# Kernel tuning notes

Hardware: AMD Instinct MI355X
Metric: run time of the kernel (lower is better)

The kernel has to match this reference:

```python
import jax, jax.numpy as jnp
import numpy as np

EPS = 1e-5

def conv3x3(x, w, b):
    # x: [B,C,H,W], w: [O,I,3,3] -> SAME padding (pad=1)
    y = jax.lax.conv_general_dilated(x, w, (1, 1), 'SAME',
                                     dimension_numbers=('NCHW', 'OIHW', 'NCHW'))
    return y + b[None, :, None, None]

def batchnorm(x, g, b):
    # training-mode batch statistics over (B,H,W), biased variance (torch default)
    m = x.mean(axis=(0, 2, 3), keepdims=True)
    v = x.var(axis=(0, 2, 3), keepdims=True)
    return (x - m) / jnp.sqrt(v + EPS) * g[None, :, None, None] + b[None, :, None, None]

def setup_inputs() -> dict:
    key = jax.random.key(0)
    ks = jax.random.split(key, 24)
    B, Cin, Cout, T, H, W = 16, 256, 256, 256, 32, 32
    Cq = Cout // 8
    s = lambda fan: 1.0 / np.sqrt(fan)
    inp = {
        'x': jax.random.normal(ks[0], (B, Cin, H, W), jnp.float32),
        't': jax.random.normal(ks[1], (B, T), jnp.float32),
        # time_mlp: Linear(T,T) -> ReLU -> Linear(T,Cout)
        'w_t1': jax.random.normal(ks[2], (T, T), jnp.float32) * s(T),
        'b_t1': jax.random.normal(ks[3], (T,), jnp.float32) * s(T),
        'w_t2': jax.random.normal(ks[4], (Cout, T), jnp.float32) * s(T),
        'b_t2': jax.random.normal(ks[5], (Cout,), jnp.float32) * s(T),
        # convs (3x3, pad=1)
        'w_c1': jax.random.normal(ks[6], (Cout, Cin, 3, 3), jnp.float32) * s(Cin * 9),
        'b_c1': jax.random.normal(ks[7], (Cout,), jnp.float32) * s(Cin * 9),
        'w_c2': jax.random.normal(ks[8], (Cout, Cout, 3, 3), jnp.float32) * s(Cout * 9),
        'b_c2': jax.random.normal(ks[9], (Cout,), jnp.float32) * s(Cout * 9),
        'w_tr': jax.random.normal(ks[10], (Cout, Cout, 3, 3), jnp.float32) * s(Cout * 9),
        'b_tr': jax.random.normal(ks[11], (Cout,), jnp.float32) * s(Cout * 9),
        # batchnorm affine params
        'bn1_g': jnp.ones((Cout,), jnp.float32),
        'bn1_b': jnp.zeros((Cout,), jnp.float32),
        'bn2_g': jnp.ones((Cout,), jnp.float32),
        'bn2_b': jnp.zeros((Cout,), jnp.float32),
        # self-attention 1x1 convs (stored as [O,I])
        'wq': jax.random.normal(ks[12], (Cq, Cout), jnp.float32) * s(Cout),
        'bq': jax.random.normal(ks[13], (Cq,), jnp.float32) * s(Cout),
        'wk': jax.random.normal(ks[14], (Cq, Cout), jnp.float32) * s(Cout),
        'bk': jax.random.normal(ks[15], (Cq,), jnp.float32) * s(Cout),
        'wv': jax.random.normal(ks[16], (Cout, Cout), jnp.float32) * s(Cout),
        'bv': jax.random.normal(ks[17], (Cout,), jnp.float32) * s(Cout),
        # gamma is nn.Parameter(zeros(1)); use a random value so the residual branch is exercised
        'gamma': jax.random.normal(ks[18], (1,), jnp.float32),
    }
    return inp

def reference(x, t, w_t1, b_t1, w_t2, b_t2, w_c1, b_c1, w_c2, b_c2, w_tr, b_tr,
              bn1_g, bn1_b, bn2_g, bn2_b, wq, bq, wk, bk, wv, bv, gamma):
    # --- Block ---
    h = batchnorm(jax.nn.relu(conv3x3(x, w_c1, b_c1)), bn1_g, bn1_b)
    te = jax.nn.relu(t @ w_t1.T + b_t1)
    te = jax.nn.relu(te @ w_t2.T + b_t2)          # [B, Cout]
    h = h + te[:, :, None, None]
    h = batchnorm(jax.nn.relu(conv3x3(h, w_c2, b_c2)), bn2_g, bn2_b)
    y = conv3x3(h, w_tr, b_tr)                    # transform (up=False)
    # --- SelfAttention ---
    B, C, H, W = y.shape
    yf = y.reshape(B, C, H * W)                   # [B, C, N]
    Q = jnp.einsum('qc,bcn->bnq', wq, yf) + bq[None, None, :]   # [B, N, Cq]
    K = jnp.einsum('qc,bcn->bqn', wk, yf) + bk[None, :, None]   # [B, Cq, N]
    V = jnp.einsum('vc,bcn->bvn', wv, yf) + bv[None, :, None]   # [B, C, N]
    attn = jax.nn.softmax(jnp.einsum('bnq,bqm->bnm', Q, K), axis=-1)  # [B, N, N]
    out = jnp.einsum('bcm,bnm->bcn', V, attn).reshape(B, C, H, W)
    return gamma[0] * out + y
```

## Files before the change

### kernel.cpp

```cpp
#include <hip/hip_runtime.h>
#include <hip/hip_bf16.h>

using bf16 = __hip_bfloat16;

typedef __attribute__((ext_vector_type(8))) short bf16x8_t;
typedef __attribute__((ext_vector_type(4))) float f32x4_t;

__device__ __forceinline__ float b2f(bf16 x){ return __bfloat162float(x); }
__device__ __forceinline__ bf16  f2b(float x){ return __float2bfloat16(x); }
__device__ __forceinline__ unsigned short f2bu(float x){ bf16 h = __float2bfloat16(x); return *(unsigned short*)&h; }
__device__ __forceinline__ float bits2f(unsigned int lo16){ return __uint_as_float(lo16 << 16); }

__device__ __forceinline__ void gload16(const void* g, void* l) {
    __builtin_amdgcn_global_load_lds(
        (const __attribute__((address_space(1))) unsigned int*)g,
        (__attribute__((address_space(3))) unsigned int*)l, 16, 0, 0);
}


__global__ void zero_k(unsigned int* __restrict__ p, unsigned int n) {
    for (unsigned int i = blockIdx.x * 256 + threadIdx.x; i < n; i += gridDim.x * 256) p[i] = 0u;
}

__global__ __launch_bounds__(256) void time_mlp_k(
    const float* __restrict__ t, const float* __restrict__ w1, const float* __restrict__ b1,
    const float* __restrict__ w2, const float* __restrict__ b2, float* __restrict__ te)
{
    const int b = blockIdx.x, j = threadIdx.x;
    __shared__ float tr[256], hid[256];
    tr[j] = t[(b << 8) + j];
    __syncthreads();
    float s = b1[j];
    const float* wp = w1 + j * 256;
    for (int k = 0; k < 256; ++k) s += tr[k] * wp[k];
    hid[j] = fmaxf(s, 0.f);
    __syncthreads();
    float s2 = b2[j];
    const float* wp2 = w2 + j * 256;
    for (int k = 0; k < 256; ++k) s2 += hid[k] * wp2[k];
    te[(b << 8) + j] = fmaxf(s2, 0.f);
}

__global__ __launch_bounds__(256) void prep_w_all_k(
    const float* __restrict__ w1, const float* __restrict__ w2, const float* __restrict__ w3,
    bf16* __restrict__ W1, bf16* __restrict__ W2, bf16* __restrict__ W3o)
{
    __shared__ float ls[2304];
    const int t = threadIdx.x;
    const int co = blockIdx.x & 255;
    const int sel = blockIdx.x >> 8;
    const float* w = (sel == 0) ? w1 : (sel == 1) ? w2 : w3;
    bf16* dst = (sel == 0) ? W1 : (sel == 1) ? W2 : W3o;
    const float* src = w + (size_t)co * 2304;
    #pragma unroll
    for (int i = 0; i < 9; ++i) ls[t + (i << 8)] = src[t + (i << 8)];
    __syncthreads();
    #pragma unroll
    for (int off = 0; off < 9; ++off)
        dst[(size_t)(co * 9 + off) * 256 + t] = f2b(ls[t * 9 + off]);
}

__global__ __launch_bounds__(256) void prep_wqkv_k(
    const float* __restrict__ wq, const float* __restrict__ wk, const float* __restrict__ wv,
    bf16* __restrict__ WQK, bf16* __restrict__ WVb)
{
    const int r = blockIdx.x, c = threadIdx.x;
    if (r < 32)       WQK[r * 256 + c] = f2b(wq[r * 256 + c]);
    else if (r < 64)  WQK[r * 256 + c] = f2b(wk[(r - 32) * 256 + c]);
    else              WVb[(r - 64) * 256 + c] = f2b(wv[(r - 64) * 256 + c]);
}

__global__ __launch_bounds__(256) void prep_x_k(const float* __restrict__ x, bf16* __restrict__ Xp,
                                                float* __restrict__ sums)
{
    __shared__ float xs[64][65];
    const int t = threadIdx.x;
    if (blockIdx.x == 0) {
        sums[t] = 0.f; sums[t + 256] = 0.f; sums[t + 512] = 0.f; sums[t + 768] = 0.f;
    }
    const int b = blockIdx.x >> 6, ct = (blockIdx.x >> 4) & 3, nt = blockIdx.x & 15;
    const int c0 = ct << 6, n0 = nt << 6;
    {
        const int cl = t >> 2, nc = (t & 3) << 4;
        const float* src = x + (size_t)((b << 8) + c0 + cl) * 1024 + n0 + nc;
        #pragma unroll
        for (int j = 0; j < 16; j += 4) {
            const float4 v = *(const float4*)(src + j);
            xs[cl][nc + j] = v.x; xs[cl][nc + j + 1] = v.y;
            xs[cl][nc + j + 2] = v.z; xs[cl][nc + j + 3] = v.w;
        }
    }
    __syncthreads();
    {
        const int nl = t >> 2, cc = (t & 3) << 4;
        const int n = n0 + nl;
        const int p = ((n >> 5) + 1) * 34 + (n & 31) + 1;
        unsigned int u[8];
        #pragma unroll
        for (int k = 0; k < 8; ++k)
            u[k] = (unsigned int)f2bu(xs[cc + 2 * k][nl]) | ((unsigned int)f2bu(xs[cc + 2 * k + 1][nl]) << 16);
        bf16* dst = Xp + (size_t)(b * 1156 + p) * 256 + c0 + cc;
        *(uint4*)dst = make_uint4(u[0], u[1], u[2], u[3]);
        *(uint4*)(dst + 8) = make_uint4(u[4], u[5], u[6], u[7]);
    }
}

template<bool RELU, bool STATS>
__global__ __launch_bounds__(512, 1) void conv_mfma_k(
    const bf16* __restrict__ Xp, const bf16* __restrict__ W3,
    const float* __restrict__ bias, bf16* __restrict__ outp, float* __restrict__ sums)
{
    __shared__ bf16 Als[3][128 * 64];
    __shared__ bf16 Bls[3][128 * 64];
    __shared__ float sstat[256];
    const int tid = threadIdx.x;
    const int wid = tid >> 6, lane = tid & 63;
    const int wm = wid >> 2, wn = wid & 3;
    const int blk = blockIdx.x;
    const int xc = blk & 7, tt = blk >> 3;
    const int b = xc + ((tt >> 4) << 3);
    const int tile = tt & 15, mt = tile >> 1, nt = tile & 1;
    const int m0 = mt << 7, co0 = nt << 7;

    if (STATS && tid < 256) sstat[tid] = 0.f;

    const int lrow = tid >> 3;
    const int sL8 = (((tid & 7) ^ (lrow & 7)) << 3);

    const bf16* agp[2]; const bf16* bgp[2];
    #pragma unroll
    for (int i = 0; i < 2; ++i) {
        const int r = (i << 6) + lrow;
        const int n = m0 + r;
        const int pb = (n >> 5) * 34 + (n & 31);
        agp[i] = Xp + (size_t)(b * 1156 + pb) * 256 + sL8;
        bgp[i] = W3 + (size_t)(co0 + r) * 2304 + sL8;
    }

    const int rsel = lane & 15;
    const int s0 = (((lane >> 4) ^ (lane & 7)) << 3);
    const int s1 = ((((lane >> 4) + 4) ^ (lane & 7)) << 3);
    const int abase = ((wm << 6) + rsel) << 6;
    const int bbase = ((wn << 5) + rsel) << 6;

    f32x4_t acc[4][2];
    #pragma unroll
    for (int mi = 0; mi < 4; ++mi)
        #pragma unroll
        for (int ni = 0; ni < 2; ++ni)
            acc[mi][ni] = (f32x4_t){0.f, 0.f, 0.f, 0.f};

    auto STAGE = [&](int kt2, int buf) {
        const int off_ = kt2 >> 2, cic_ = kt2 & 3;
        const int kh_ = (off_ * 11) >> 5;
        const int doff_ = ((off_ + 31 * kh_) << 8) + (cic_ << 6);
        const int koff_ = (off_ << 8) + (cic_ << 6);
        #pragma unroll
        for (int i = 0; i < 2; ++i) {
            gload16(agp[i] + doff_, &Als[buf][((i << 6) + (wid << 3)) << 6]);
            gload16(bgp[i] + koff_, &Bls[buf][((i << 6) + (wid << 3)) << 6]);
        }
    };

    STAGE(0, 0); STAGE(1, 1);
    for (int kt = 0; kt < 36; ++kt) {
        if (kt < 35) asm volatile("s_waitcnt vmcnt(4)" ::: "memory");
        else         asm volatile("s_waitcnt vmcnt(0)" ::: "memory");
        __builtin_amdgcn_s_barrier();
        asm volatile("" ::: "memory");
        const int cur = kt % 3;
        #pragma unroll
        for (int kh = 0; kh < 2; ++kh) {
            const int sk = kh ? s1 : s0;
            bf16x8_t av[4], bv[2];
            #pragma unroll
            for (int mi = 0; mi < 4; ++mi)
                av[mi] = *(const bf16x8_t*)(&Als[cur][abase + (mi << 10) + sk]);
            #pragma unroll
            for (int ni = 0; ni < 2; ++ni)
                bv[ni] = *(const bf16x8_t*)(&Bls[cur][bbase + (ni << 10) + sk]);
            #pragma unroll
            for (int mi = 0; mi < 4; ++mi)
                #pragma unroll
                for (int ni = 0; ni < 2; ++ni)
                    acc[mi][ni] = __builtin_amdgcn_mfma_f32_16x16x32_bf16(
                        av[mi], bv[ni], acc[mi][ni], 0, 0, 0);
        }
        if (kt + 2 < 36) STAGE(kt + 2, (kt + 2) % 3);
    }

    const int cr = (lane >> 4) << 2;
    const int cc = lane & 15;
    #pragma unroll
    for (int ni = 0; ni < 2; ++ni) {
        const int co = co0 + (wn << 5) + (ni << 4) + cc;
        const float bb = bias[co];
        float ssum = 0.f, ssq = 0.f;
        #pragma unroll
        for (int mi = 0; mi < 4; ++mi) {
            const int n = m0 + (wm << 6) + (mi << 4) + cr;
            #pragma unroll
            for (int j = 0; j < 4; ++j) {
                float v = acc[mi][ni][j] + bb;
                if (RELU) v = fmaxf(v, 0.f);
                outp[(size_t)((b << 10) + n + j) * 256 + co] = f2b(v);
                if (STATS) { ssum += v; ssq += v * v; }
            }
        }
        if (STATS) {
            ssum += __shfl_xor(ssum, 16); ssum += __shfl_xor(ssum, 32);
            ssq  += __shfl_xor(ssq, 16);  ssq  += __shfl_xor(ssq, 32);
            if (lane < 16) {
                const int ch = (wn << 5) + (ni << 4) + cc;
                atomicAdd(&sstat[ch * 2], ssum);
                atomicAdd(&sstat[ch * 2 + 1], ssq);
            }
        }
    }
    if (STATS) {
        __syncthreads();
        if (tid < 128) {
            atomicAdd(&sums[co0 + tid], sstat[tid * 2]);
            atomicAdd(&sums[256 + co0 + tid], sstat[tid * 2 + 1]);
        }
    }
}

template<bool TE>
__global__ __launch_bounds__(256) void bn_apply_T_k(
    const bf16* __restrict__ a, const float* __restrict__ sums,
    const float* __restrict__ g, const float* __restrict__ bb,
    const float* __restrict__ te, bf16* __restrict__ Xp)
{
    const int t = threadIdx.x;
    const int row = blockIdx.x * 8 + (t >> 5);
    const int c0 = (t & 31) << 3;
    const int b = row >> 10, n = row & 1023;
    const uint4 u = *(const uint4*)(a + (size_t)row * 256 + c0);
    const unsigned int w[4] = {u.x, u.y, u.z, u.w};
    float scv[8], shv[8];
    #pragma unroll
    for (int k = 0; k < 8; ++k) {
        const int c = c0 + k;
        const float m = sums[c] * (1.f / 16384.f);
        const float var = sums[256 + c] * (1.f / 16384.f) - m * m;
        const float sc = g[c] * rsqrtf(var + 1e-5f);
        scv[k] = sc;
        shv[k] = bb[c] - m * sc + (TE ? te[(b << 8) + c] : 0.f);
    }
    unsigned int o[4];
    #pragma unroll
    for (int k = 0; k < 4; ++k) {
        const float v0 = bits2f(w[k] & 0xffffu) * scv[2*k] + shv[2*k];
        const float v1 = __uint_as_float(w[k] & 0xffff0000u) * scv[2*k+1] + shv[2*k+1];
        o[k] = (unsigned int)f2bu(v0) | ((unsigned int)f2bu(v1) << 16);
    }
    const int p = ((n >> 5) + 1) * 34 + (n & 31) + 1;
    *(uint4*)(Xp + (size_t)(b * 1156 + p) * 256 + c0) = make_uint4(o[0], o[1], o[2], o[3]);
}

__global__ __launch_bounds__(256) void qk_mfma_k(
    const bf16* __restrict__ Yt, const bf16* __restrict__ WQK,
    const float* __restrict__ bq, const float* __restrict__ bk, bf16* __restrict__ QKb)
{
    const int b = blockIdx.x >> 4, m0 = (blockIdx.x & 15) << 6;
    const int tid = threadIdx.x, wid = tid >> 6, lane = tid & 63;
    const int n0w = m0 + (wid << 4);
    const bf16* arow = Yt + (size_t)((b << 10) + n0w + (lane & 15)) * 256 + ((lane >> 4) << 3);
    const int boff = ((lane >> 4) << 3);
    f32x4_t acc[4];
    #pragma unroll
    for (int ni = 0; ni < 4; ++ni) acc[ni] = (f32x4_t){0.f,0.f,0.f,0.f};
    for (int k0 = 0; k0 < 256; k0 += 32) {
        const bf16x8_t av = *(const bf16x8_t*)(arow + k0);
        #pragma unroll
        for (int ni = 0; ni < 4; ++ni) {
            const bf16x8_t bv = *(const bf16x8_t*)(WQK + (ni * 16 + (lane & 15)) * 256 + k0 + boff);
            acc[ni] = __builtin_amdgcn_mfma_f32_16x16x32_bf16(av, bv, acc[ni], 0, 0, 0);
        }
    }
    const int cr = (lane >> 4) << 2, cc = lane & 15;
    #pragma unroll
    for (int ni = 0; ni < 4; ++ni) {
        const int q = ni * 16 + cc;
        const float bias = (q < 32) ? bq[q] : bk[q - 32];
        #pragma unroll
        for (int j = 0; j < 4; ++j) {
            const int n = n0w + cr + j;
            QKb[(size_t)((b << 10) + n) * 64 + q] = f2b(acc[ni][j] + bias);
        }
    }
}

__global__ __launch_bounds__(512, 1) void v_mfma_k(
    const bf16* __restrict__ WVb, const bf16* __restrict__ Yt,
    const float* __restrict__ bvp, bf16* __restrict__ Vb)
{
    __shared__ bf16 Als[3][128 * 64];
    __shared__ bf16 Bls[3][128 * 64];
    const int tid = threadIdx.x;
    const int wid = tid >> 6, lane = tid & 63;
    const int wm = wid >> 2, wn = wid & 3;
    const int blk = blockIdx.x;
    const int xc = blk & 7, tt = blk >> 3;
    const int b = xc + ((tt >> 4) << 3);
    const int tile = tt & 15, vt = tile >> 3, nt = tile & 7;
    const int v0 = vt << 7, n0 = nt << 7;

    const int lrow = tid >> 3;
    const int sL8 = (((tid & 7) ^ (lrow & 7)) << 3);
    const bf16* agp[2]; const bf16* bgp[2];
    #pragma unroll
    for (int i = 0; i < 2; ++i) {
        const int r = (i << 6) + lrow;
        agp[i] = WVb + (size_t)(v0 + r) * 256 + sL8;
        bgp[i] = Yt + (size_t)((b << 10) + n0 + r) * 256 + sL8;
    }
    const int rsel = lane & 15;
    const int s0 = (((lane >> 4) ^ (lane & 7)) << 3);
    const int s1 = ((((lane >> 4) + 4) ^ (lane & 7)) << 3);
    const int abase = ((wm << 6) + rsel) << 6;
    const int bbase = ((wn << 5) + rsel) << 6;

    f32x4_t acc[4][2];
    #pragma unroll
    for (int mi = 0; mi < 4; ++mi)
        #pragma unroll
        for (int ni = 0; ni < 2; ++ni)
            acc[mi][ni] = (f32x4_t){0.f,0.f,0.f,0.f};

    auto STAGE = [&](int kt2, int buf) {
        const int koff = kt2 << 6;
        #pragma unroll
        for (int i = 0; i < 2; ++i) {
            gload16(agp[i] + koff, &Als[buf][((i << 6) + (wid << 3)) << 6]);
            gload16(bgp[i] + koff, &Bls[buf][((i << 6) + (wid << 3)) << 6]);
        }
    };

    STAGE(0, 0); STAGE(1, 1);
    for (int kt = 0; kt < 4; ++kt) {
        if (kt < 3) asm volatile("s_waitcnt vmcnt(4)" ::: "memory");
        else        asm volatile("s_waitcnt vmcnt(0)" ::: "memory");
        __builtin_amdgcn_s_barrier();
        asm volatile("" ::: "memory");
        const int cur = kt % 3;
        #pragma unroll
        for (int kh = 0; kh < 2; ++kh) {
            const int sk = kh ? s1 : s0;
            bf16x8_t av[4], bv[2];
            #pragma unroll
            for (int mi = 0; mi < 4; ++mi)
                av[mi] = *(const bf16x8_t*)(&Als[cur][abase + (mi << 10) + sk]);
            #pragma unroll
            for (int ni = 0; ni < 2; ++ni)
                bv[ni] = *(const bf16x8_t*)(&Bls[cur][bbase + (ni << 10) + sk]);
            #pragma unroll
            for (int mi = 0; mi < 4; ++mi)
                #pragma unroll
                for (int ni = 0; ni < 2; ++ni)
                    acc[mi][ni] = __builtin_amdgcn_mfma_f32_16x16x32_bf16(
                        av[mi], bv[ni], acc[mi][ni], 0, 0, 0);
        }
        if (kt + 2 < 4) STAGE(kt + 2, (kt + 2) % 3);
    }

    const int cr = (lane >> 4) << 2, cc = lane & 15;
    #pragma unroll
    for (int mi = 0; mi < 4; ++mi) {
        #pragma unroll
        for (int j = 0; j < 4; ++j) {
            const int v = v0 + (wm << 6) + (mi << 4) + cr + j;
            const float bb = bvp[v];
            #pragma unroll
            for (int ni = 0; ni < 2; ++ni) {
                const int n = n0 + (wn << 5) + (ni << 4) + cc;
                Vb[(size_t)((b << 8) + v) * 1024 + n] = f2b(acc[mi][ni][j] + bb);
            }
        }
    }
}

__global__ __launch_bounds__(256) void softmax_k(
    const bf16* __restrict__ QKb, bf16* __restrict__ P, float* __restrict__ invs)
{
    const int b = blockIdx.x >> 5, n0 = (blockIdx.x & 31) << 5;
    const int tid = threadIdx.x, wid = tid >> 6, lane = tid & 63;
    const int m0w = wid << 8;
    __shared__ float wred[4][32];

    const bf16* qbase = QKb + (size_t)((b << 10) + n0) * 64;
    const int koff = (lane >> 4) << 3;
    bf16x8_t qf[2];
    #pragma unroll
    for (int nt = 0; nt < 2; ++nt)
        qf[nt] = *(const bf16x8_t*)(qbase + (nt * 16 + (lane & 15)) * 64 + koff);
    const bf16* kbase = QKb + (size_t)(b << 10) * 64 + 32;

    float mx[2] = {-3.0e38f, -3.0e38f};
    for (int mi = 0; mi < 16; ++mi) {
        const bf16x8_t kf = *(const bf16x8_t*)(kbase + (m0w + mi * 16 + (lane & 15)) * 64 + koff);
        #pragma unroll
        for (int nt = 0; nt < 2; ++nt) {
            f32x4_t s = (f32x4_t){0.f,0.f,0.f,0.f};
            s = __builtin_amdgcn_mfma_f32_16x16x32_bf16(kf, qf[nt], s, 0, 0, 0);
            mx[nt] = fmaxf(mx[nt], fmaxf(fmaxf(s[0], s[1]), fmaxf(s[2], s[3])));
        }
    }
    #pragma unroll
    for (int nt = 0; nt < 2; ++nt) {
        mx[nt] = fmaxf(mx[nt], __shfl_xor(mx[nt], 16));
        mx[nt] = fmaxf(mx[nt], __shfl_xor(mx[nt], 32));
        if (lane < 16) wred[wid][nt * 16 + lane] = mx[nt];
    }
    __syncthreads();
    float rm[2];
    #pragma unroll
    for (int nt = 0; nt < 2; ++nt) {
        const int c = nt * 16 + (lane & 15);
        rm[nt] = fmaxf(fmaxf(wred[0][c], wred[1][c]), fmaxf(wred[2][c], wred[3][c]));
    }
    __syncthreads();

    float sm[2] = {0.f, 0.f};
    for (int mi = 0; mi < 16; ++mi) {
        const bf16x8_t kf = *(const bf16x8_t*)(kbase + (m0w + mi * 16 + (lane & 15)) * 64 + koff);
        #pragma unroll
        for (int nt = 0; nt < 2; ++nt) {
            f32x4_t s = (f32x4_t){0.f,0.f,0.f,0.f};
            s = __builtin_amdgcn_mfma_f32_16x16x32_bf16(kf, qf[nt], s, 0, 0, 0);
            const float p0 = __expf(s[0] - rm[nt]);
            const float p1 = __expf(s[1] - rm[nt]);
            const float p2 = __expf(s[2] - rm[nt]);
            const float p3 = __expf(s[3] - rm[nt]);
            sm[nt] += (p0 + p1) + (p2 + p3);
            uint2 u;
            u.x = (unsigned int)f2bu(p0) | ((unsigned int)f2bu(p1) << 16);
            u.y = (unsigned int)f2bu(p2) | ((unsigned int)f2bu(p3) << 16);
            const int n = n0 + nt * 16 + (lane & 15);
            const int m = m0w + mi * 16 + ((lane >> 4) << 2);
            *(uint2*)(P + (size_t)((b << 10) + n) * 1024 + m) = u;
        }
    }
    #pragma unroll
    for (int nt = 0; nt < 2; ++nt) {
        sm[nt] += __shfl_xor(sm[nt], 16);
        sm[nt] += __shfl_xor(sm[nt], 32);
        if (lane < 16) wred[wid][nt * 16 + lane] = sm[nt];
    }
    __syncthreads();
    if (tid < 32) {
        const float total = wred[0][tid] + wred[1][tid] + wred[2][tid] + wred[3][tid];
        invs[(b << 10) + n0 + tid] = 1.f / total;
    }
}

__global__ __launch_bounds__(512, 1) void pv_mfma_k(
    const bf16* __restrict__ Vb, const bf16* __restrict__ P,
    const float* __restrict__ invs, const bf16* __restrict__ Yt,
    const float* __restrict__ gamma, float* __restrict__ out)
{
    __shared__ bf16 Als[3][128 * 64];
    __shared__ bf16 Bls[3][128 * 64];
    const int tid = threadIdx.x;
    const int wid = tid >> 6, lane = tid & 63;
    const int wm = wid >> 2, wn = wid & 3;
    const int blk = blockIdx.x;
    const int xc = blk & 7, tt = blk >> 3;
    const int b = xc + ((tt >> 4) << 3);
    const int tile = tt & 15, ct = tile >> 3, nt = tile & 7;
    const int c0 = ct << 7, n0 = nt << 7;

    const int lrow = tid >> 3;
    const int sL8 = (((tid & 7) ^ (lrow & 7)) << 3);
    const bf16* agp[2]; const bf16* bgp[2];
    #pragma unroll
    for (int i = 0; i < 2; ++i) {
        const int r = (i << 6) + lrow;
        agp[i] = Vb + (size_t)((b << 8) + c0 + r) * 1024 + sL8;
        bgp[i] = P + (size_t)((b << 10) + n0 + r) * 1024 + sL8;
    }
    const int rsel = lane & 15;
    const int s0 = (((lane >> 4) ^ (lane & 7)) << 3);
    const int s1 = ((((lane >> 4) + 4) ^ (lane & 7)) << 3);
    const int abase = ((wm << 6) + rsel) << 6;
    const int bbase = ((wn << 5) + rsel) << 6;

    f32x4_t acc[4][2];
    #pragma unroll
    for (int mi = 0; mi < 4; ++mi)
        #pragma unroll
        for (int ni = 0; ni < 2; ++ni)
            acc[mi][ni] = (f32x4_t){0.f,0.f,0.f,0.f};

    auto STAGE = [&](int kt2, int buf) {
        const int koff = kt2 << 6;
        #pragma unroll
        for (int i = 0; i < 2; ++i) {
            gload16(agp[i] + koff, &Als[buf][((i << 6) + (wid << 3)) << 6]);
            gload16(bgp[i] + koff, &Bls[buf][((i << 6) + (wid << 3)) << 6]);
        }
    };

    STAGE(0, 0); STAGE(1, 1);
    for (int kt = 0; kt < 16; ++kt) {
        if (kt < 15) asm volatile("s_waitcnt vmcnt(4)" ::: "memory");
        else         asm volatile("s_waitcnt vmcnt(0)" ::: "memory");
        __builtin_amdgcn_s_barrier();
        asm volatile("" ::: "memory");
        const int cur = kt % 3;
        #pragma unroll
        for (int kh = 0; kh < 2; ++kh) {
            const int sk = kh ? s1 : s0;
            bf16x8_t av[4], bv[2];
            #pragma unroll
            for (int mi = 0; mi < 4; ++mi)
                av[mi] = *(const bf16x8_t*)(&Als[cur][abase + (mi << 10) + sk]);
            #pragma unroll
            for (int ni = 0; ni < 2; ++ni)
                bv[ni] = *(const bf16x8_t*)(&Bls[cur][bbase + (ni << 10) + sk]);
            #pragma unroll
            for (int mi = 0; mi < 4; ++mi)
                #pragma unroll
                for (int ni = 0; ni < 2; ++ni)
                    acc[mi][ni] = __builtin_amdgcn_mfma_f32_16x16x32_bf16(
                        av[mi], bv[ni], acc[mi][ni], 0, 0, 0);
        }
        if (kt + 2 < 16) STAGE(kt + 2, (kt + 2) % 3);
    }

    const float g = gamma[0];
    const int cr = (lane >> 4) << 2, cc = lane & 15;
    #pragma unroll
    for (int ni = 0; ni < 2; ++ni) {
        const int n = n0 + (wn << 5) + (ni << 4) + cc;
        const float gi = g * invs[(b << 10) + n];
        #pragma unroll
        for (int mi = 0; mi < 4; ++mi) {
            const int c = c0 + (wm << 6) + (mi << 4) + cr;
            const bf16* yp = Yt + (size_t)((b << 10) + n) * 256 + c;
            #pragma unroll
            for (int j = 0; j < 4; ++j)
                out[(size_t)((b << 8) + c + j) * 1024 + n] = gi * acc[mi][ni][j] + b2f(yp[j]);
        }
    }
}

extern "C" void kernel_launch(void* const* d_in, const int* in_sizes, int n_in,
                              void* d_out, int out_size, void* d_ws, size_t ws_size,
                              hipStream_t stream)
{
    const float* x     = (const float*)d_in[0];
    const float* t     = (const float*)d_in[1];
    const float* w_t1  = (const float*)d_in[2];
    const float* b_t1  = (const float*)d_in[3];
    const float* w_t2  = (const float*)d_in[4];
    const float* b_t2  = (const float*)d_in[5];
    const float* w_c1  = (const float*)d_in[6];
    const float* b_c1  = (const float*)d_in[7];
    const float* w_c2  = (const float*)d_in[8];
    const float* b_c2  = (const float*)d_in[9];
    const float* w_tr  = (const float*)d_in[10];
    const float* b_tr  = (const float*)d_in[11];
    const float* bn1g  = (const float*)d_in[12];
    const float* bn1b  = (const float*)d_in[13];
    const float* bn2g  = (const float*)d_in[14];
    const float* bn2b  = (const float*)d_in[15];
    const float* wq    = (const float*)d_in[16];
    const float* bq    = (const float*)d_in[17];
    const float* wk    = (const float*)d_in[18];
    const float* bk    = (const float*)d_in[19];
    const float* wv    = (const float*)d_in[20];
    const float* bv    = (const float*)d_in[21];
    const float* gamma = (const float*)d_in[22];
    float* out = (float*)d_out;

    char* ws = (char*)d_ws;
    float* te    = (float*)(ws + 0);
    float* sums1 = (float*)(ws + 16384);
    float* sums2 = (float*)(ws + 18432);
    char* base = ws + 32768;
    bf16* W3_1 = (bf16*)(base);
    bf16* W3_2 = (bf16*)(base + 1179648);
    bf16* W3_3 = (bf16*)(base + 2359296);
    bf16* Xp0  = (bf16*)(base + 3538944);
    bf16* Xp1  = (bf16*)(base + 13008896);
    bf16* Craw = (bf16*)(base + 22478848);
    bf16* P    = (bf16*)(base);
    bf16* Yt   = (bf16*)(base + 33554432);
    bf16* QKb  = (bf16*)(base + 41943040);
    bf16* Vb   = (bf16*)(base + 44040192);
    float* invs= (float*)(base + 52428800);
    bf16* WQK  = (bf16*)(base + 52494336);
    bf16* WVb  = (bf16*)(base + 52527104);

    const unsigned int XP2_U32 = 2u * 16u * 1156u * 256u / 2u;

    zero_k<<<2048, 256, 0, stream>>>((unsigned int*)Xp0, XP2_U32);
    time_mlp_k<<<16, 256, 0, stream>>>(t, w_t1, b_t1, w_t2, b_t2, te);
    prep_w_all_k<<<768, 256, 0, stream>>>(w_c1, w_c2, w_tr, W3_1, W3_2, W3_3);
    prep_wqkv_k<<<320, 256, 0, stream>>>(wq, wk, wv, WQK, WVb);
    prep_x_k<<<1024, 256, 0, stream>>>(x, Xp0, sums1);

    conv_mfma_k<true, true><<<256, 512, 0, stream>>>(Xp0, W3_1, b_c1, Craw, sums1);
    bn_apply_T_k<true><<<2048, 256, 0, stream>>>(Craw, sums1, bn1g, bn1b, te, Xp1);

    conv_mfma_k<true, true><<<256, 512, 0, stream>>>(Xp1, W3_2, b_c2, Craw, sums2);
    bn_apply_T_k<false><<<2048, 256, 0, stream>>>(Craw, sums2, bn2g, bn2b, nullptr, Xp0);

    conv_mfma_k<false, false><<<256, 512, 0, stream>>>(Xp0, W3_3, b_tr, Yt, nullptr);

    qk_mfma_k<<<256, 256, 0, stream>>>(Yt, WQK, bq, bk, QKb);
    v_mfma_k<<<256, 512, 0, stream>>>(WVb, Yt, bv, Vb);
    softmax_k<<<512, 256, 0, stream>>>(QKb, P, invs);
    pv_mfma_k<<<256, 512, 0, stream>>>(Vb, P, invs, Yt, gamma, out);
}
```

Baseline: 169.7 us.

## Fuse softmax and PV matmul into flash-style online-softmax attention kernel

Replaces the separate softmax kernel, which wrote the full BxNxN probability matrix to global memory, and the PV matmul that read it back, with one kernel using online softmax. Each wave recomputes QK^T scores per 64-key chunk, rescales its running accumulator, stages probabilities through per-wave LDS and feeds them to MFMA against V loaded straight from global. This removes the P round trip (about 32MB of bf16) and one launch. In exchange, QK scores are recomputed by every channel-tile block (two C tiles per n tile), V is read from global without LDS staging or prefetch, and the exp and rescale work adds VALU load.

```diff
diff --git a/kernel.cpp b/kernel.cpp
--- a/kernel.cpp
+++ b/kernel.cpp
@@ -381,163 +381,139 @@
     }
 }
 
-__global__ __launch_bounds__(256) void softmax_k(
-    const bf16* __restrict__ QKb, bf16* __restrict__ P, float* __restrict__ invs)
-{
-    const int b = blockIdx.x >> 5, n0 = (blockIdx.x & 31) << 5;
-    const int tid = threadIdx.x, wid = tid >> 6, lane = tid & 63;
-    const int m0w = wid << 8;
-    __shared__ float wred[4][32];
-
-    const bf16* qbase = QKb + (size_t)((b << 10) + n0) * 64;
-    const int koff = (lane >> 4) << 3;
-    bf16x8_t qf[2];
-    #pragma unroll
-    for (int nt = 0; nt < 2; ++nt)
-        qf[nt] = *(const bf16x8_t*)(qbase + (nt * 16 + (lane & 15)) * 64 + koff);
-    const bf16* kbase = QKb + (size_t)(b << 10) * 64 + 32;
-
-    float mx[2] = {-3.0e38f, -3.0e38f};
-    for (int mi = 0; mi < 16; ++mi) {
-        const bf16x8_t kf = *(const bf16x8_t*)(kbase + (m0w + mi * 16 + (lane & 15)) * 64 + koff);
-        #pragma unroll
-        for (int nt = 0; nt < 2; ++nt) {
-            f32x4_t s = (f32x4_t){0.f,0.f,0.f,0.f};
-            s = __builtin_amdgcn_mfma_f32_16x16x32_bf16(kf, qf[nt], s, 0, 0, 0);
-            mx[nt] = fmaxf(mx[nt], fmaxf(fmaxf(s[0], s[1]), fmaxf(s[2], s[3])));
-        }
-    }
-    #pragma unroll
-    for (int nt = 0; nt < 2; ++nt) {
-        mx[nt] = fmaxf(mx[nt], __shfl_xor(mx[nt], 16));
-        mx[nt] = fmaxf(mx[nt], __shfl_xor(mx[nt], 32));
-        if (lane < 16) wred[wid][nt * 16 + lane] = mx[nt];
-    }
-    __syncthreads();
-    float rm[2];
-    #pragma unroll
-    for (int nt = 0; nt < 2; ++nt) {
-        const int c = nt * 16 + (lane & 15);
-        rm[nt] = fmaxf(fmaxf(wred[0][c], wred[1][c]), fmaxf(wred[2][c], wred[3][c]));
-    }
-    __syncthreads();
-
-    float sm[2] = {0.f, 0.f};
-    for (int mi = 0; mi < 16; ++mi) {
-        const bf16x8_t kf = *(const bf16x8_t*)(kbase + (m0w + mi * 16 + (lane & 15)) * 64 + koff);
-        #pragma unroll
-        for (int nt = 0; nt < 2; ++nt) {
-            f32x4_t s = (f32x4_t){0.f,0.f,0.f,0.f};
-            s = __builtin_amdgcn_mfma_f32_16x16x32_bf16(kf, qf[nt], s, 0, 0, 0);
-            const float p0 = __expf(s[0] - rm[nt]);
-            const float p1 = __expf(s[1] - rm[nt]);
-            const float p2 = __expf(s[2] - rm[nt]);
-            const float p3 = __expf(s[3] - rm[nt]);
-            sm[nt] += (p0 + p1) + (p2 + p3);
-            uint2 u;
-            u.x = (unsigned int)f2bu(p0) | ((unsigned int)f2bu(p1) << 16);
-            u.y = (unsigned int)f2bu(p2) | ((unsigned int)f2bu(p3) << 16);
-            const int n = n0 + nt * 16 + (lane & 15);
-            const int m = m0w + mi * 16 + ((lane >> 4) << 2);
-            *(uint2*)(P + (size_t)((b << 10) + n) * 1024 + m) = u;
-        }
-    }
-    #pragma unroll
-    for (int nt = 0; nt < 2; ++nt) {
-        sm[nt] += __shfl_xor(sm[nt], 16);
-        sm[nt] += __shfl_xor(sm[nt], 32);
-        if (lane < 16) wred[wid][nt * 16 + lane] = sm[nt];
-    }
-    __syncthreads();
-    if (tid < 32) {
-        const float total = wred[0][tid] + wred[1][tid] + wred[2][tid] + wred[3][tid];
-        invs[(b << 10) + n0 + tid] = 1.f / total;
-    }
-}
-
-__global__ __launch_bounds__(512, 1) void pv_mfma_k(
-    const bf16* __restrict__ Vb, const bf16* __restrict__ P,
-    const float* __restrict__ invs, const bf16* __restrict__ Yt,
-    const float* __restrict__ gamma, float* __restrict__ out)
-{
-    __shared__ bf16 Als[3][128 * 64];
-    __shared__ bf16 Bls[3][128 * 64];
+__global__ __launch_bounds__(512, 2) void attn_fused_k(
+    const bf16* __restrict__ QKb, const bf16* __restrict__ Vb,
+    const bf16* __restrict__ Yt, const float* __restrict__ gamma, float* __restrict__ out)
+{
+    __shared__ bf16 S_lds[8][2048];
     const int tid = threadIdx.x;
     const int wid = tid >> 6, lane = tid & 63;
+    const int l15 = lane & 15, lg = lane >> 4;
     const int wm = wid >> 2, wn = wid & 3;
     const int blk = blockIdx.x;
     const int xc = blk & 7, tt = blk >> 3;
     const int b = xc + ((tt >> 4) << 3);
     const int tile = tt & 15, ct = tile >> 3, nt = tile & 7;
-    const int c0 = ct << 7, n0 = nt << 7;
-
-    const int lrow = tid >> 3;
-    const int sL8 = (((tid & 7) ^ (lrow & 7)) << 3);
-    const bf16* agp[2]; const bf16* bgp[2];
-    #pragma unroll
-    for (int i = 0; i < 2; ++i) {
-        const int r = (i << 6) + lrow;
-        agp[i] = Vb + (size_t)((b << 8) + c0 + r) * 1024 + sL8;
-        bgp[i] = P + (size_t)((b << 10) + n0 + r) * 1024 + sL8;
-    }
-    const int rsel = lane & 15;
-    const int s0 = (((lane >> 4) ^ (lane & 7)) << 3);
-    const int s1 = ((((lane >> 4) + 4) ^ (lane & 7)) << 3);
-    const int abase = ((wm << 6) + rsel) << 6;
-    const int bbase = ((wn << 5) + rsel) << 6;
-
+    const int c0w = (ct << 7) + (wm << 6);
+    const int n0w = (nt << 7) + (wn << 5);
+
+    bf16* sl = S_lds[wid];
+    const int e0 = (l15 & 7) << 1;
+
+    bf16x8_t qf[2];
+    #pragma unroll
+    for (int ni = 0; ni < 2; ++ni)
+        qf[ni] = *(const bf16x8_t*)(QKb + (size_t)((b << 10) + n0w + ni * 16 + l15) * 64 + (lg << 3));
+
+    float m_run[2] = {-3.0e38f, -3.0e38f};
+    float s_run[2] = {0.f, 0.f};
     f32x4_t acc[4][2];
     #pragma unroll
     for (int mi = 0; mi < 4; ++mi)
         #pragma unroll
         for (int ni = 0; ni < 2; ++ni)
-            acc[mi][ni] = (f32x4_t){0.f,0.f,0.f,0.f};
-
-    auto STAGE = [&](int kt2, int buf) {
-        const int koff = kt2 << 6;
-        #pragma unroll
-        for (int i = 0; i < 2; ++i) {
-            gload16(agp[i] + koff, &Als[buf][((i << 6) + (wid << 3)) << 6]);
-            gload16(bgp[i] + koff, &Bls[buf][((i << 6) + (wid << 3)) << 6]);
-        }
-    };
-
-    STAGE(0, 0); STAGE(1, 1);
-    for (int kt = 0; kt < 16; ++kt) {
-        if (kt < 15) asm volatile("s_waitcnt vmcnt(4)" ::: "memory");
-        else         asm volatile("s_waitcnt vmcnt(0)" ::: "memory");
-        __builtin_amdgcn_s_barrier();
-        asm volatile("" ::: "memory");
-        const int cur = kt % 3;
-        #pragma unroll
-        for (int kh = 0; kh < 2; ++kh) {
-            const int sk = kh ? s1 : s0;
-            bf16x8_t av[4], bv[2];
-            #pragma unroll
-            for (int mi = 0; mi < 4; ++mi)
-                av[mi] = *(const bf16x8_t*)(&Als[cur][abase + (mi << 10) + sk]);
-            #pragma unroll
-            for (int ni = 0; ni < 2; ++ni)
-                bv[ni] = *(const bf16x8_t*)(&Bls[cur][bbase + (ni << 10) + sk]);
+            acc[mi][ni] = (f32x4_t){0.f, 0.f, 0.f, 0.f};
+
+    const bf16* kbase = QKb + (size_t)(b << 10) * 64 + 32 + (lg << 3);
+    const bf16* vbase = Vb + (size_t)((b << 8) + c0w) * 1024 + (lg << 3);
+
+    for (int m0 = 0; m0 < 1024; m0 += 64) {
+        bf16x8_t kf[4], av[4][2];
+        #pragma unroll
+        for (int mi = 0; mi < 4; ++mi)
+            kf[mi] = *(const bf16x8_t*)(kbase + (size_t)(m0 + mi * 16 + l15) * 64);
+        #pragma unroll
+        for (int mi = 0; mi < 4; ++mi)
+            #pragma unroll
+            for (int ms = 0; ms < 2; ++ms)
+                av[mi][ms] = *(const bf16x8_t*)(vbase + (size_t)(mi * 16 + l15) * 1024 + m0 + ms * 32);
+
+        f32x4_t s[4][2];
+        #pragma unroll
+        for (int mi = 0; mi < 4; ++mi)
+            #pragma unroll
+            for (int ni = 0; ni < 2; ++ni) {
+                f32x4_t z = (f32x4_t){0.f, 0.f, 0.f, 0.f};
+                s[mi][ni] = __builtin_amdgcn_mfma_f32_16x16x32_bf16(kf[mi], qf[ni], z, 0, 0, 0);
+            }
+
+        #pragma unroll
+        for (int ni = 0; ni < 2; ++ni) {
+            float tm = s[0][ni][0];
+            #pragma unroll
+            for (int mi = 0; mi < 4; ++mi)
+                #pragma unroll
+                for (int j = 0; j < 4; ++j) tm = fmaxf(tm, s[mi][ni][j]);
+            tm = fmaxf(tm, __shfl_xor(tm, 16));
+            tm = fmaxf(tm, __shfl_xor(tm, 32));
+            const float nm = fmaxf(m_run[ni], tm);
+            const float f = __expf(m_run[ni] - nm);
+            m_run[ni] = nm;
+            #pragma unroll
+            for (int mi = 0; mi < 4; ++mi)
+                #pragma unroll
+                for (int j = 0; j < 4; ++j) acc[mi][ni][j] *= f;
+            float ls = 0.f;
+            #pragma unroll
+            for (int mi = 0; mi < 4; ++mi)
+                #pragma unroll
+                for (int j = 0; j < 4; ++j) {
+                    const float p = __expf(s[mi][ni][j] - nm);
+                    s[mi][ni][j] = p;
+                    ls += p;
+                }
+            ls += __shfl_xor(ls, 16);
+            ls += __shfl_xor(ls, 32);
+            s_run[ni] = s_run[ni] * f + ls;
+        }
+
+        #pragma unroll
+        for (int ni = 0; ni < 2; ++ni) {
+            const int n_local = ni * 16 + l15;
+            const int rowb = n_local << 7;
+            #pragma unroll
+            for (int mi = 0; mi < 4; ++mi) {
+                const int pg = ((mi << 2) + lg) ^ e0;
+                uint2 u;
+                u.x = (unsigned int)f2bu(s[mi][ni][0]) | ((unsigned int)f2bu(s[mi][ni][1]) << 16);
+                u.y = (unsigned int)f2bu(s[mi][ni][2]) | ((unsigned int)f2bu(s[mi][ni][3]) << 16);
+                *(uint2*)((char*)sl + rowb + (pg << 3)) = u;
+            }
+        }
+        asm volatile("s_waitcnt lgkmcnt(0)" ::: "memory");
+        __builtin_amdgcn_sched_barrier(0);
+
+        bf16x8_t bv[2][2];
+        #pragma unroll
+        for (int ni = 0; ni < 2; ++ni) {
+            const int n_local = ni * 16 + l15;
+            const int rowb = n_local << 7;
+            #pragma unroll
+            for (int ms = 0; ms < 2; ++ms) {
+                const int pg = ((ms << 3) + (lg << 1)) ^ e0;
+                bv[ni][ms] = *(const bf16x8_t*)((const char*)sl + rowb + (pg << 3));
+            }
+        }
+
+        #pragma unroll
+        for (int ms = 0; ms < 2; ++ms)
             #pragma unroll
             for (int mi = 0; mi < 4; ++mi)
                 #pragma unroll
                 for (int ni = 0; ni < 2; ++ni)
                     acc[mi][ni] = __builtin_amdgcn_mfma_f32_16x16x32_bf16(
-                        av[mi], bv[ni], acc[mi][ni], 0, 0, 0);
-        }
-        if (kt + 2 < 16) STAGE(kt + 2, (kt + 2) % 3);
+                        av[mi][ms], bv[ni][ms], acc[mi][ni], 0, 0, 0);
+        asm volatile("" ::: "memory");
     }
 
     const float g = gamma[0];
-    const int cr = (lane >> 4) << 2, cc = lane & 15;
     #pragma unroll
     for (int ni = 0; ni < 2; ++ni) {
-        const int n = n0 + (wn << 5) + (ni << 4) + cc;
-        const float gi = g * invs[(b << 10) + n];
+        const int n = n0w + ni * 16 + l15;
+        const float gi = g / s_run[ni];
         #pragma unroll
         for (int mi = 0; mi < 4; ++mi) {
-            const int c = c0 + (wm << 6) + (mi << 4) + cr;
+            const int c = c0w + mi * 16 + (lg << 2);
             const bf16* yp = Yt + (size_t)((b << 10) + n) * 256 + c;
             #pragma unroll
             for (int j = 0; j < 4; ++j)
@@ -586,11 +562,9 @@
     bf16* Xp0  = (bf16*)(base + 3538944);
     bf16* Xp1  = (bf16*)(base + 13008896);
     bf16* Craw = (bf16*)(base + 22478848);
-    bf16* P    = (bf16*)(base);
     bf16* Yt   = (bf16*)(base + 33554432);
     bf16* QKb  = (bf16*)(base + 41943040);
     bf16* Vb   = (bf16*)(base + 44040192);
-    float* invs= (float*)(base + 52428800);
     bf16* WQK  = (bf16*)(base + 52494336);
     bf16* WVb  = (bf16*)(base + 52527104);
 
@@ -612,6 +586,5 @@
 
     qk_mfma_k<<<256, 256, 0, stream>>>(Yt, WQK, bq, bk, QKb);
     v_mfma_k<<<256, 512, 0, stream>>>(WVb, Yt, bv, Vb);
-    softmax_k<<<512, 256, 0, stream>>>(QKb, P, invs);
-    pv_mfma_k<<<256, 512, 0, stream>>>(Vb, P, invs, Yt, gamma, out);
-}
+    attn_fused_k<<<256, 512, 0, stream>>>(QKb, Vb, Yt, gamma, out);
+}
```

After: 184.3 us. 1.09x slower.

## Merge prep kernels into one launch, zero only halo borders, fuse QK and V projections

Applied to the files above, without the earlier changes.

Folds the zeroing, time-MLP, weight conversion, QKV weight prep and input transpose into a single block-dispatched prep kernel. The full zeroing of both padded buffers is replaced by writes to only the halo border rows. The QK and V projection kernels are merged into one launch, with extra blocks doing QK at 512 threads. This cuts launch count and memory traffic, but it relies on the interior of Xp1 always being fully overwritten, and the QK blocks now carry the large shared-memory allocation of the V path, which may lower occupancy.

```diff
diff --git a/kernel.cpp b/kernel.cpp
--- a/kernel.cpp
+++ b/kernel.cpp
@@ -18,90 +18,101 @@
 }
 
 
-__global__ void zero_k(unsigned int* __restrict__ p, unsigned int n) {
-    for (unsigned int i = blockIdx.x * 256 + threadIdx.x; i < n; i += gridDim.x * 256) p[i] = 0u;
-}
-
-__global__ __launch_bounds__(256) void time_mlp_k(
-    const float* __restrict__ t, const float* __restrict__ w1, const float* __restrict__ b1,
-    const float* __restrict__ w2, const float* __restrict__ b2, float* __restrict__ te)
-{
-    const int b = blockIdx.x, j = threadIdx.x;
-    __shared__ float tr[256], hid[256];
-    tr[j] = t[(b << 8) + j];
-    __syncthreads();
-    float s = b1[j];
-    const float* wp = w1 + j * 256;
-    for (int k = 0; k < 256; ++k) s += tr[k] * wp[k];
-    hid[j] = fmaxf(s, 0.f);
-    __syncthreads();
-    float s2 = b2[j];
-    const float* wp2 = w2 + j * 256;
-    for (int k = 0; k < 256; ++k) s2 += hid[k] * wp2[k];
-    te[(b << 8) + j] = fmaxf(s2, 0.f);
-}
-
-__global__ __launch_bounds__(256) void prep_w_all_k(
+__global__ __launch_bounds__(256) void prep_all_k(
+    const float* __restrict__ x, bf16* __restrict__ Xp0, bf16* __restrict__ Xp1,
+    float* __restrict__ sums,
+    const float* __restrict__ t, const float* __restrict__ w_t1, const float* __restrict__ b_t1,
+    const float* __restrict__ w_t2, const float* __restrict__ b_t2, float* __restrict__ te,
     const float* __restrict__ w1, const float* __restrict__ w2, const float* __restrict__ w3,
-    bf16* __restrict__ W1, bf16* __restrict__ W2, bf16* __restrict__ W3o)
-{
-    __shared__ float ls[2304];
-    const int t = threadIdx.x;
-    const int co = blockIdx.x & 255;
-    const int sel = blockIdx.x >> 8;
-    const float* w = (sel == 0) ? w1 : (sel == 1) ? w2 : w3;
-    bf16* dst = (sel == 0) ? W1 : (sel == 1) ? W2 : W3o;
-    const float* src = w + (size_t)co * 2304;
-    #pragma unroll
-    for (int i = 0; i < 9; ++i) ls[t + (i << 8)] = src[t + (i << 8)];
-    __syncthreads();
-    #pragma unroll
-    for (int off = 0; off < 9; ++off)
-        dst[(size_t)(co * 9 + off) * 256 + t] = f2b(ls[t * 9 + off]);
-}
-
-__global__ __launch_bounds__(256) void prep_wqkv_k(
+    bf16* __restrict__ W1, bf16* __restrict__ W2, bf16* __restrict__ W3o,
     const float* __restrict__ wq, const float* __restrict__ wk, const float* __restrict__ wv,
     bf16* __restrict__ WQK, bf16* __restrict__ WVb)
 {
-    const int r = blockIdx.x, c = threadIdx.x;
-    if (r < 32)       WQK[r * 256 + c] = f2b(wq[r * 256 + c]);
-    else if (r < 64)  WQK[r * 256 + c] = f2b(wk[(r - 32) * 256 + c]);
-    else              WVb[(r - 64) * 256 + c] = f2b(wv[(r - 64) * 256 + c]);
-}
-
-__global__ __launch_bounds__(256) void prep_x_k(const float* __restrict__ x, bf16* __restrict__ Xp,
-                                                float* __restrict__ sums)
-{
-    __shared__ float xs[64][65];
-    const int t = threadIdx.x;
-    if (blockIdx.x == 0) {
-        sums[t] = 0.f; sums[t + 256] = 0.f; sums[t + 512] = 0.f; sums[t + 768] = 0.f;
-    }
-    const int b = blockIdx.x >> 6, ct = (blockIdx.x >> 4) & 3, nt = blockIdx.x & 15;
-    const int c0 = ct << 6, n0 = nt << 6;
-    {
-        const int cl = t >> 2, nc = (t & 3) << 4;
-        const float* src = x + (size_t)((b << 8) + c0 + cl) * 1024 + n0 + nc;
-        #pragma unroll
-        for (int j = 0; j < 16; j += 4) {
-            const float4 v = *(const float4*)(src + j);
-            xs[cl][nc + j] = v.x; xs[cl][nc + j + 1] = v.y;
-            xs[cl][nc + j + 2] = v.z; xs[cl][nc + j + 3] = v.w;
-        }
-    }
-    __syncthreads();
-    {
-        const int nl = t >> 2, cc = (t & 3) << 4;
-        const int n = n0 + nl;
-        const int p = ((n >> 5) + 1) * 34 + (n & 31) + 1;
-        unsigned int u[8];
-        #pragma unroll
-        for (int k = 0; k < 8; ++k)
-            u[k] = (unsigned int)f2bu(xs[cc + 2 * k][nl]) | ((unsigned int)f2bu(xs[cc + 2 * k + 1][nl]) << 16);
-        bf16* dst = Xp + (size_t)(b * 1156 + p) * 256 + c0 + cc;
-        *(uint4*)dst = make_uint4(u[0], u[1], u[2], u[3]);
-        *(uint4*)(dst + 8) = make_uint4(u[4], u[5], u[6], u[7]);
+    __shared__ char smem[64 * 65 * 4];
+    const int blk = blockIdx.x;
+    const int tid = threadIdx.x;
+
+    if (blk < 1024) {
+        float (*xs)[65] = (float(*)[65])smem;
+        if (blk == 0) {
+            sums[tid] = 0.f; sums[tid + 256] = 0.f; sums[tid + 512] = 0.f; sums[tid + 768] = 0.f;
+        }
+        const int b = blk >> 6, ct = (blk >> 4) & 3, nt = blk & 15;
+        const int c0 = ct << 6, n0 = nt << 6;
+        {
+            const int cl = tid >> 2, nc = (tid & 3) << 4;
+            const float* src = x + (size_t)((b << 8) + c0 + cl) * 1024 + n0 + nc;
+            #pragma unroll
+            for (int j = 0; j < 16; j += 4) {
+                const float4 v = *(const float4*)(src + j);
+                xs[cl][nc + j] = v.x; xs[cl][nc + j + 1] = v.y;
+                xs[cl][nc + j + 2] = v.z; xs[cl][nc + j + 3] = v.w;
+            }
+        }
+        __syncthreads();
+        {
+            const int nl = tid >> 2, cc = (tid & 3) << 4;
+            const int n = n0 + nl;
+            const int p = ((n >> 5) + 1) * 34 + (n & 31) + 1;
+            unsigned int u[8];
+            #pragma unroll
+            for (int k = 0; k < 8; ++k)
+                u[k] = (unsigned int)f2bu(xs[cc + 2 * k][nl]) | ((unsigned int)f2bu(xs[cc + 2 * k + 1][nl]) << 16);
+            bf16* dst = Xp0 + (size_t)(b * 1156 + p) * 256 + c0 + cc;
+            *(uint4*)dst = make_uint4(u[0], u[1], u[2], u[3]);
+            *(uint4*)(dst + 8) = make_uint4(u[4], u[5], u[6], u[7]);
+        }
+    } else if (blk < 1792) {
+        float* ls = (float*)smem;
+        const int id = blk - 1024;
+        const int co = id & 255;
+        const int sel = id >> 8;
+        const float* w = (sel == 0) ? w1 : (sel == 1) ? w2 : w3;
+        bf16* dst = (sel == 0) ? W1 : (sel == 1) ? W2 : W3o;
+        const float* src = w + (size_t)co * 2304;
+        #pragma unroll
+        for (int i = 0; i < 9; ++i) ls[tid + (i << 8)] = src[tid + (i << 8)];
+        __syncthreads();
+        #pragma unroll
+        for (int off = 0; off < 9; ++off)
+            dst[(size_t)(co * 9 + off) * 256 + tid] = f2b(ls[tid * 9 + off]);
+    } else if (blk < 2112) {
+        const int r = blk - 1792;
+        if (r < 32)       WQK[r * 256 + tid] = f2b(wq[r * 256 + tid]);
+        else if (r < 64)  WQK[r * 256 + tid] = f2b(wk[(r - 32) * 256 + tid]);
+        else              WVb[(r - 64) * 256 + tid] = f2b(wv[(r - 64) * 256 + tid]);
+    } else if (blk < 2128) {
+        float* tr = (float*)smem;
+        float* hid = tr + 256;
+        const int b = blk - 2112, j = tid;
+        tr[j] = t[(b << 8) + j];
+        __syncthreads();
+        float s = b_t1[j];
+        const float* wp = w_t1 + j * 256;
+        for (int k = 0; k < 256; ++k) s += tr[k] * wp[k];
+        hid[j] = fmaxf(s, 0.f);
+        __syncthreads();
+        float s2 = b_t2[j];
+        const float* wp2 = w_t2 + j * 256;
+        for (int k = 0; k < 256; ++k) s2 += hid[k] * wp2[k];
+        te[(b << 8) + j] = fmaxf(s2, 0.f);
+    } else {
+        const int idx = (blk - 2128) * 256 + tid;
+        const int v = idx >> 6;
+        const int o = (idx & 63) << 1;
+        if (v < 4224) {
+            const int buf = v / 2112;
+            const int rem = v - buf * 2112;
+            const int b = rem / 132;
+            const int h = rem - b * 132;
+            int p;
+            if (h < 34)        p = h;
+            else if (h < 68)   p = 1122 + (h - 34);
+            else if (h < 100)  p = (h - 68 + 1) * 34;
+            else               p = (h - 100 + 1) * 34 + 33;
+            unsigned int* dst = (unsigned int*)((buf ? Xp1 : Xp0) + (size_t)(b * 1156 + p) * 256);
+            dst[o] = 0u; dst[o + 1] = 0u;
+        }
     }
 }
 
@@ -259,47 +270,48 @@
     *(uint4*)(Xp + (size_t)(b * 1156 + p) * 256 + c0) = make_uint4(o[0], o[1], o[2], o[3]);
 }
 
-__global__ __launch_bounds__(256) void qk_mfma_k(
-    const bf16* __restrict__ Yt, const bf16* __restrict__ WQK,
-    const float* __restrict__ bq, const float* __restrict__ bk, bf16* __restrict__ QKb)
-{
-    const int b = blockIdx.x >> 4, m0 = (blockIdx.x & 15) << 6;
-    const int tid = threadIdx.x, wid = tid >> 6, lane = tid & 63;
-    const int n0w = m0 + (wid << 4);
-    const bf16* arow = Yt + (size_t)((b << 10) + n0w + (lane & 15)) * 256 + ((lane >> 4) << 3);
-    const int boff = ((lane >> 4) << 3);
-    f32x4_t acc[4];
-    #pragma unroll
-    for (int ni = 0; ni < 4; ++ni) acc[ni] = (f32x4_t){0.f,0.f,0.f,0.f};
-    for (int k0 = 0; k0 < 256; k0 += 32) {
-        const bf16x8_t av = *(const bf16x8_t*)(arow + k0);
-        #pragma unroll
-        for (int ni = 0; ni < 4; ++ni) {
-            const bf16x8_t bv = *(const bf16x8_t*)(WQK + (ni * 16 + (lane & 15)) * 256 + k0 + boff);
-            acc[ni] = __builtin_amdgcn_mfma_f32_16x16x32_bf16(av, bv, acc[ni], 0, 0, 0);
-        }
-    }
-    const int cr = (lane >> 4) << 2, cc = lane & 15;
-    #pragma unroll
-    for (int ni = 0; ni < 4; ++ni) {
-        const int q = ni * 16 + cc;
-        const float bias = (q < 32) ? bq[q] : bk[q - 32];
-        #pragma unroll
-        for (int j = 0; j < 4; ++j) {
-            const int n = n0w + cr + j;
-            QKb[(size_t)((b << 10) + n) * 64 + q] = f2b(acc[ni][j] + bias);
-        }
-    }
-}
-
-__global__ __launch_bounds__(512, 1) void v_mfma_k(
+__global__ __launch_bounds__(512, 1) void qkv_mfma_k(
     const bf16* __restrict__ WVb, const bf16* __restrict__ Yt,
-    const float* __restrict__ bvp, bf16* __restrict__ Vb)
+    const float* __restrict__ bvp, bf16* __restrict__ Vb,
+    const bf16* __restrict__ WQK, const float* __restrict__ bq,
+    const float* __restrict__ bk, bf16* __restrict__ QKb)
 {
     __shared__ bf16 Als[3][128 * 64];
     __shared__ bf16 Bls[3][128 * 64];
     const int tid = threadIdx.x;
     const int wid = tid >> 6, lane = tid & 63;
+
+    if (blockIdx.x >= 256) {
+        const int blk2 = blockIdx.x - 256;
+        const int b = blk2 >> 3, m0 = (blk2 & 7) << 7;
+        const int n0w = m0 + (wid << 4);
+        const bf16* arow = Yt + (size_t)((b << 10) + n0w + (lane & 15)) * 256 + ((lane >> 4) << 3);
+        const int boff = ((lane >> 4) << 3);
+        f32x4_t acc[4];
+        #pragma unroll
+        for (int ni = 0; ni < 4; ++ni) acc[ni] = (f32x4_t){0.f,0.f,0.f,0.f};
+        for (int k0 = 0; k0 < 256; k0 += 32) {
+            const bf16x8_t av = *(const bf16x8_t*)(arow + k0);
+            #pragma unroll
+            for (int ni = 0; ni < 4; ++ni) {
+                const bf16x8_t bv = *(const bf16x8_t*)(WQK + (ni * 16 + (lane & 15)) * 256 + k0 + boff);
+                acc[ni] = __builtin_amdgcn_mfma_f32_16x16x32_bf16(av, bv, acc[ni], 0, 0, 0);
+            }
+        }
+        const int cr = (lane >> 4) << 2, cc = lane & 15;
+        #pragma unroll
+        for (int ni = 0; ni < 4; ++ni) {
+            const int q = ni * 16 + cc;
+            const float bias = (q < 32) ? bq[q] : bk[q - 32];
+            #pragma unroll
+            for (int j = 0; j < 4; ++j) {
+                const int n = n0w + cr + j;
+                QKb[(size_t)((b << 10) + n) * 64 + q] = f2b(acc[ni][j] + bias);
+            }
+        }
+        return;
+    }
+
     const int wm = wid >> 2, wn = wid & 3;
     const int blk = blockIdx.x;
     const int xc = blk & 7, tt = blk >> 3;
@@ -594,13 +606,11 @@
     bf16* WQK  = (bf16*)(base + 52494336);
     bf16* WVb  = (bf16*)(base + 52527104);
 
-    const unsigned int XP2_U32 = 2u * 16u * 1156u * 256u / 2u;
-
-    zero_k<<<2048, 256, 0, stream>>>((unsigned int*)Xp0, XP2_U32);
-    time_mlp_k<<<16, 256, 0, stream>>>(t, w_t1, b_t1, w_t2, b_t2, te);
-    prep_w_all_k<<<768, 256, 0, stream>>>(w_c1, w_c2, w_tr, W3_1, W3_2, W3_3);
-    prep_wqkv_k<<<320, 256, 0, stream>>>(wq, wk, wv, WQK, WVb);
-    prep_x_k<<<1024, 256, 0, stream>>>(x, Xp0, sums1);
+    prep_all_k<<<3184, 256, 0, stream>>>(
+        x, Xp0, Xp1, sums1,
+        t, w_t1, b_t1, w_t2, b_t2, te,
+        w_c1, w_c2, w_tr, W3_1, W3_2, W3_3,
+        wq, wk, wv, WQK, WVb);
 
     conv_mfma_k<true, true><<<256, 512, 0, stream>>>(Xp0, W3_1, b_c1, Craw, sums1);
     bn_apply_T_k<true><<<2048, 256, 0, stream>>>(Craw, sums1, bn1g, bn1b, te, Xp1);
@@ -610,8 +620,7 @@
 
     conv_mfma_k<false, false><<<256, 512, 0, stream>>>(Xp0, W3_3, b_tr, Yt, nullptr);
 
-    qk_mfma_k<<<256, 256, 0, stream>>>(Yt, WQK, bq, bk, QKb);
-    v_mfma_k<<<256, 512, 0, stream>>>(WVb, Yt, bv, Vb);
+    qkv_mfma_k<<<384, 512, 0, stream>>>(WVb, Yt, bv, Vb, WQK, bq, bk, QKb);
     softmax_k<<<512, 256, 0, stream>>>(QKb, P, invs);
     pv_mfma_k<<<256, 512, 0, stream>>>(Vb, P, invs, Yt, gamma, out);
 }
```

New measurement: 158.4 us. 6.7% less time.
